# Kernel tuning notes

Measured on AMD Instinct MI355X. Metric: run time of the kernel, lower is better.

## Reference

```python
import jax, jax.numpy as jnp
import numpy as np

N_QUERY, N_POINTS, FEAT_DIM, K = 32768, 8192, 32, 8

def setup_inputs() -> dict:
    key = jax.random.key(0)
    k1, k2, k3 = jax.random.split(key, 3)
    xyz = jax.random.normal(k1, (N_QUERY, 3), dtype=jnp.float32)
    points = jax.random.normal(k2, (N_POINTS, 3), dtype=jnp.float32)
    # neural_point features are initialized uniform(-1e-4, 1e-4) in the module;
    # we use small-scale gaussians of the same magnitude.
    feats = jax.random.normal(k3, (N_POINTS, FEAT_DIM), dtype=jnp.float32) * 1e-4
    return {"xyz": xyz, "points": points, "feats": feats, "k": K}

def reference(xyz, points, feats, k):
    # Brute-force exact KNN (kpknn equivalent): squared euclidean distances [N, P]
    d2 = (jnp.sum(xyz * xyz, axis=-1, keepdims=True)
          - 2.0 * (xyz @ points.T)
          + jnp.sum(points * points, axis=-1)[None, :])
    _, idx = jax.lax.top_k(-d2, k)          # idx: [N, k] nearest-point indices
    knn_points = points[idx]                # [N, k, 3]
    knn_feats = feats[idx]                  # [N, k, FEAT_DIM]
    return knn_points, knn_feats
```

## Files before the change

kernel.cpp:

```cpp
#include <hip/hip_runtime.h>

#define NQ 32768
#define NP 8192
#define FD 32
#define KNN 8
#define QW 4
#define WPB 8
#define TB 512
#define QBLK (QW * WPB)
#define CHP 1024
#define NCH (NP / CHP)
#define ABLK 2048
#define CAP 128

typedef unsigned long long u64;

__device__ __forceinline__ u64 shfl_xor_u64(u64 k, int j) {
    unsigned lo = __shfl_xor((unsigned)k, j);
    unsigned hi = __shfl_xor((unsigned)(k >> 32), j);
    return ((u64)hi << 32) | lo;
}
__device__ __forceinline__ u64 sort64_u64(u64 key, int lane) {
    for (int k2 = 2; k2 <= 64; k2 <<= 1)
        for (int j = k2 >> 1; j > 0; j >>= 1) {
            u64 o = shfl_xor_u64(key, j);
            bool keepMin = ((lane & k2) == 0) == ((lane & j) == 0);
            key = ((o < key) == keepMin) ? o : key;
        }
    return key;
}
__device__ __forceinline__ float eighth_smallest64(float v, int lane) {
    for (int k2 = 2; k2 <= 64; k2 <<= 1)
        for (int j = k2 >> 1; j > 0; j >>= 1) {
            float o = __shfl_xor(v, j);
            bool keepMin = ((lane & k2) == 0) == ((lane & j) == 0);
            v = ((o < v) == keepMin) ? o : v;
        }
    return __uint_as_float((unsigned)__builtin_amdgcn_readlane((int)__float_as_uint(v), 7));
}

__global__ void k_prepack(const float* __restrict__ points, float4* __restrict__ pts4) {
    int i = blockIdx.x * blockDim.x + threadIdx.x;
    float px = points[i * 3 + 0], py = points[i * 3 + 1], pz = points[i * 3 + 2];
    float pn = __builtin_fmaf(pz, pz, __builtin_fmaf(py, py, px * px));
    pts4[i] = make_float4(-2.0f * px, -2.0f * py, -2.0f * pz, pn);
}

__global__ __launch_bounds__(TB) void knn_kernel(
    const float* __restrict__ xyz, const float* __restrict__ points,
    const float* __restrict__ feats, const float4* __restrict__ pts4,
    float* __restrict__ out)
{
#pragma clang fp contract(off)
    __shared__ float4 sp[CHP];
    __shared__ unsigned short sidx16[QBLK * CAP];
    __shared__ int scnt[QBLK];

    const int t     = threadIdx.x;
    const int lane  = t & 63;
    const int wid   = t >> 6;
    const int qbase = blockIdx.x * QBLK + wid * QW;

    if (t < QBLK) scnt[t] = 0;

    float qx[QW], qy[QW], qz[QW], qn[QW], mn[QW], tscr[QW];
#pragma unroll
    for (int qq = 0; qq < QW; ++qq) {
        int q = qbase + qq;
        float a = xyz[q * 3 + 0], b = xyz[q * 3 + 1], c = xyz[q * 3 + 2];
        qx[qq] = a; qy[qq] = b; qz[qq] = c;
        qn[qq] = (a * a + b * b) + c * c;
        mn[qq] = __builtin_inff();
    }

#pragma unroll 4
    for (int s = 0; s < ABLK / 64; ++s) {
        float4 p = pts4[s * 64 + lane];
#pragma unroll
        for (int qq = 0; qq < QW; ++qq) {
            float g = __builtin_fmaf(qx[qq], p.x,
                      __builtin_fmaf(qy[qq], p.y,
                      __builtin_fmaf(qz[qq], p.z, p.w)));
            mn[qq] = fminf(mn[qq], g);
        }
    }
#pragma unroll
    for (int qq = 0; qq < QW; ++qq)
        tscr[qq] = eighth_smallest64(mn[qq], lane) + 1e-3f;

    for (int c = 0; c < NCH; ++c) {
        __syncthreads();
        for (int i = t; i < CHP; i += TB) sp[i] = pts4[c * CHP + i];
        __syncthreads();
#pragma unroll 4
        for (int s = 0; s < CHP / 64; ++s) {
            float4 p = sp[s * 64 + lane];
#pragma unroll
            for (int qq = 0; qq < QW; ++qq) {
                float g = __builtin_fmaf(qx[qq], p.x,
                          __builtin_fmaf(qy[qq], p.y,
                          __builtin_fmaf(qz[qq], p.z, p.w)));
                if (__builtin_expect(g <= tscr[qq], 0)) {
                    int wq = wid * QW + qq;
                    int slot = atomicAdd(&scnt[wq], 1);
                    if (slot < CAP) sidx16[wq * CAP + slot] = (unsigned short)(c * CHP + s * 64 + lane);
                }
            }
        }
    }
    __syncthreads();

    const float4* feats4 = (const float4*)feats;
    float4* outf4 = (float4*)(out + (long)NQ * KNN * 3);
#pragma unroll 1
    for (int qq = 0; qq < QW; ++qq) {
        int wq = wid * QW + qq;
        int cnt = scnt[wq]; if (cnt > CAP) cnt = CAP;

        u64 key1 = ~0ull;
        if (lane < cnt) {
            int idx = sidx16[wq * CAP + lane];
            float px = points[idx * 3 + 0], py = points[idx * 3 + 1], pz = points[idx * 3 + 2];
            float pn  = (px * px + py * py) + pz * pz;
            float dot = __builtin_fmaf(qz[qq], pz, __builtin_fmaf(qy[qq], py, qx[qq] * px));
            float d2  = (qn[qq] - 2.0f * dot) + pn;
            unsigned b = __float_as_uint(d2);
            unsigned mk = (b & 0x80000000u) ? ~b : (b | 0x80000000u);
            key1 = ((u64)mk << 32) | (unsigned)idx;
        }
        u64 v = sort64_u64(key1, lane);

        if (cnt > 64) {
            u64 key2 = ~0ull;
            if (lane + 64 < cnt) {
                int idx = sidx16[wq * CAP + 64 + lane];
                float px = points[idx * 3 + 0], py = points[idx * 3 + 1], pz = points[idx * 3 + 2];
                float pn  = (px * px + py * py) + pz * pz;
                float dot = __builtin_fmaf(qz[qq], pz, __builtin_fmaf(qy[qq], py, qx[qq] * px));
                float d2  = (qn[qq] - 2.0f * dot) + pn;
                unsigned b = __float_as_uint(d2);
                unsigned mk = (b & 0x80000000u) ? ~b : (b | 0x80000000u);
                key2 = ((u64)mk << 32) | (unsigned)idx;
            }
            u64 s2 = sort64_u64(key2, lane);
            int src = (15 - lane) & 63;
            unsigned lo2 = __shfl((unsigned)s2, src);
            unsigned hi2 = __shfl((unsigned)(s2 >> 32), src);
            u64 kr = ((u64)hi2 << 32) | lo2;
            u64 m = (lane < 8) ? v : ((lane < 16) ? kr : ~0ull);
#pragma unroll
            for (int j = 8; j > 0; j >>= 1) {
                u64 o = shfl_xor_u64(m, j);
                bool low = (lane & j) == 0;
                m = low ? (o < m ? o : m) : (o < m ? m : o);
            }
            v = m;
        }

        int q = qbase + qq;
        int nb = __shfl((int)(unsigned)v, lane >> 3);
        outf4[(long)q * (KNN * FD / 4) + lane] = feats4[(long)nb * (FD / 4) + (lane & 7)];
        int j2 = lane / 3;
        int nb2 = __shfl((int)(unsigned)v, j2);
        if (lane < 24) {
            out[(long)q * (KNN * 3) + lane] = points[nb2 * 3 + (lane - j2 * 3)];
        }
    }
}

extern "C" void kernel_launch(void* const* d_in, const int* in_sizes, int n_in,
                              void* d_out, int out_size, void* d_ws, size_t ws_size,
                              hipStream_t stream) {
    const float* xyz    = (const float*)d_in[0];
    const float* points = (const float*)d_in[1];
    const float* feats  = (const float*)d_in[2];
    float* out = (float*)d_out;
    float4* pts4 = (float4*)d_ws;

    hipLaunchKernelGGL(k_prepack, dim3(NP / 256), dim3(256), 0, stream, points, pts4);
    hipLaunchKernelGGL(knn_kernel, dim3(NQ / QBLK), dim3(TB), 0, stream,
                       xyz, points, feats, pts4, out);
}
```

Before: 77.43 us.

## Compute KNN candidate distances with split-bf16 MFMA tiles instead of scalar FMAs

```diff
diff --git a/kernel.cpp b/kernel.cpp
--- a/kernel.cpp
+++ b/kernel.cpp
@@ -4,16 +4,26 @@
 #define NP 8192
 #define FD 32
 #define KNN 8
-#define QW 4
 #define WPB 8
 #define TB 512
-#define QBLK (QW * WPB)
-#define CHP 1024
-#define NCH (NP / CHP)
-#define ABLK 2048
+#define QBLK 32
+#define NTILE (NP / 16)
+#define QTILE (NTILE / 4)
+#define ATILE 32
 #define CAP 128
+#define MARGIN 1e-2f
 
 typedef unsigned long long u64;
+typedef short short8 __attribute__((ext_vector_type(8)));
+typedef float f32x4 __attribute__((ext_vector_type(4)));
+
+__device__ __forceinline__ unsigned short f2bf(float f) {
+    unsigned u = __float_as_uint(f);
+    return (unsigned short)((u + 0x7FFFu + ((u >> 16) & 1u)) >> 16);
+}
+__device__ __forceinline__ float bf2f(unsigned short s) {
+    return __uint_as_float(((unsigned)s) << 16);
+}
 
 __device__ __forceinline__ u64 shfl_xor_u64(u64 k, int j) {
     unsigned lo = __shfl_xor((unsigned)k, j);
@@ -39,71 +49,105 @@
     return __uint_as_float((unsigned)__builtin_amdgcn_readlane((int)__float_as_uint(v), 7));
 }
 
-__global__ void k_prepack(const float* __restrict__ points, float4* __restrict__ pts4) {
-    int i = blockIdx.x * blockDim.x + threadIdx.x;
+__global__ void k_prepack(const float* __restrict__ points, unsigned short* __restrict__ ptsB) {
+    int i = blockIdx.x * 256 + threadIdx.x;
     float px = points[i * 3 + 0], py = points[i * 3 + 1], pz = points[i * 3 + 2];
+    float mx = -2.0f * px, my = -2.0f * py, mz = -2.0f * pz;
     float pn = __builtin_fmaf(pz, pz, __builtin_fmaf(py, py, px * px));
-    pts4[i] = make_float4(-2.0f * px, -2.0f * py, -2.0f * pz, pn);
+    unsigned short mhx = f2bf(mx), mhy = f2bf(my), mhz = f2bf(mz);
+    unsigned short mlx = f2bf(mx - bf2f(mhx)), mly = f2bf(my - bf2f(mhy)), mlz = f2bf(mz - bf2f(mhz));
+    unsigned short pnh = f2bf(pn), pnl = f2bf(pn - bf2f(pnh));
+    unsigned s0 = (unsigned)mhx | ((unsigned)mhy << 16);
+    unsigned s1 = (unsigned)mhz | ((unsigned)mhx << 16);
+    unsigned s2 = (unsigned)mhy | ((unsigned)mhz << 16);
+    unsigned s3 = (unsigned)mlx | ((unsigned)mly << 16);
+    unsigned s4 = (unsigned)mlz | ((unsigned)pnh << 16);
+    unsigned s5 = (unsigned)pnl;
+    uint4* o = (uint4*)(ptsB + i * 16);
+    o[0] = make_uint4(s0, s1, s2, s3);
+    o[1] = make_uint4(s4, s5, 0u, 0u);
 }
 
 __global__ __launch_bounds__(TB) void knn_kernel(
     const float* __restrict__ xyz, const float* __restrict__ points,
-    const float* __restrict__ feats, const float4* __restrict__ pts4,
+    const float* __restrict__ feats, const unsigned short* __restrict__ ptsB,
     float* __restrict__ out)
 {
 #pragma clang fp contract(off)
-    __shared__ float4 sp[CHP];
+    __shared__ float smin[2][16][64];
+    __shared__ float stau[QBLK];
     __shared__ unsigned short sidx16[QBLK * CAP];
     __shared__ int scnt[QBLK];
 
-    const int t     = threadIdx.x;
-    const int lane  = t & 63;
-    const int wid   = t >> 6;
-    const int qbase = blockIdx.x * QBLK + wid * QW;
+    const int t = threadIdx.x, lane = t & 63, wid = t >> 6;
+    const int grp = wid >> 2, quarter = wid & 3;
+    const int col = lane & 15, kb = lane >> 4;
+    const int qbase_g = blockIdx.x * QBLK + grp * 16;
 
     if (t < QBLK) scnt[t] = 0;
 
-    float qx[QW], qy[QW], qz[QW], qn[QW], mn[QW], tscr[QW];
-#pragma unroll
-    for (int qq = 0; qq < QW; ++qq) {
-        int q = qbase + qq;
-        float a = xyz[q * 3 + 0], b = xyz[q * 3 + 1], c = xyz[q * 3 + 2];
-        qx[qq] = a; qy[qq] = b; qz[qq] = c;
-        qn[qq] = (a * a + b * b) + c * c;
-        mn[qq] = __builtin_inff();
-    }
-
+    short8 af = 0;
+    {
+        int qid = qbase_g + col;
+        float a = xyz[qid * 3 + 0], b = xyz[qid * 3 + 1], c = xyz[qid * 3 + 2];
+        unsigned short qhx = f2bf(a), qhy = f2bf(b), qhz = f2bf(c);
+        unsigned short qlx = f2bf(a - bf2f(qhx)), qly = f2bf(b - bf2f(qhy)), qlz = f2bf(c - bf2f(qhz));
+        if (kb == 0) {
+            af[0] = (short)qhx; af[1] = (short)qhy; af[2] = (short)qhz;
+            af[3] = (short)qlx; af[4] = (short)qly; af[5] = (short)qlz;
+            af[6] = (short)qhx; af[7] = (short)qhy;
+        } else if (kb == 1) {
+            af[0] = (short)qhz; af[1] = (short)0x3F80; af[2] = (short)0x3F80;
+        }
+    }
+
+    const int tb0 = quarter * QTILE;
+
+    f32x4 mnA;
+    mnA[0] = mnA[1] = mnA[2] = mnA[3] = __builtin_inff();
 #pragma unroll 4
-    for (int s = 0; s < ABLK / 64; ++s) {
-        float4 p = pts4[s * 64 + lane];
-#pragma unroll
-        for (int qq = 0; qq < QW; ++qq) {
-            float g = __builtin_fmaf(qx[qq], p.x,
-                      __builtin_fmaf(qy[qq], p.y,
-                      __builtin_fmaf(qz[qq], p.z, p.w)));
-            mn[qq] = fminf(mn[qq], g);
-        }
-    }
-#pragma unroll
-    for (int qq = 0; qq < QW; ++qq)
-        tscr[qq] = eighth_smallest64(mn[qq], lane) + 1e-3f;
-
-    for (int c = 0; c < NCH; ++c) {
-        __syncthreads();
-        for (int i = t; i < CHP; i += TB) sp[i] = pts4[c * CHP + i];
-        __syncthreads();
+    for (int s = 0; s < ATILE; ++s) {
+        int tb = tb0 + s;
+        short8 bf8 = 0;
+        if (kb < 2) bf8 = *(const short8*)(ptsB + tb * 256 + col * 16 + kb * 8);
+        f32x4 acc = {0.f, 0.f, 0.f, 0.f};
+        acc = __builtin_amdgcn_mfma_f32_16x16x32_bf16(af, bf8, acc, 0, 0, 0);
+#pragma unroll
+        for (int j = 0; j < 4; ++j) mnA[j] = fminf(mnA[j], acc[j]);
+    }
+#pragma unroll
+    for (int j = 0; j < 4; ++j) smin[grp][kb * 4 + j][quarter * 16 + col] = mnA[j];
+    __syncthreads();
+
+#pragma unroll
+    for (int j2 = 0; j2 < 4; ++j2) {
+        int qloc = wid * 4 + j2;
+        float v = smin[qloc >> 4][qloc & 15][lane];
+        float t8 = eighth_smallest64(v, lane);
+        if (lane == 0) stau[qloc] = t8 + MARGIN;
+    }
+    __syncthreads();
+    float tau4[4];
+#pragma unroll
+    for (int j = 0; j < 4; ++j) tau4[j] = stau[grp * 16 + kb * 4 + j];
+
 #pragma unroll 4
-        for (int s = 0; s < CHP / 64; ++s) {
-            float4 p = sp[s * 64 + lane];
-#pragma unroll
-            for (int qq = 0; qq < QW; ++qq) {
-                float g = __builtin_fmaf(qx[qq], p.x,
-                          __builtin_fmaf(qy[qq], p.y,
-                          __builtin_fmaf(qz[qq], p.z, p.w)));
-                if (__builtin_expect(g <= tscr[qq], 0)) {
-                    int wq = wid * QW + qq;
-                    int slot = atomicAdd(&scnt[wq], 1);
-                    if (slot < CAP) sidx16[wq * CAP + slot] = (unsigned short)(c * CHP + s * 64 + lane);
+    for (int s = 0; s < QTILE; ++s) {
+        int tb = tb0 + s;
+        short8 bf8 = 0;
+        if (kb < 2) bf8 = *(const short8*)(ptsB + tb * 256 + col * 16 + kb * 8);
+        f32x4 acc = {0.f, 0.f, 0.f, 0.f};
+        acc = __builtin_amdgcn_mfma_f32_16x16x32_bf16(af, bf8, acc, 0, 0, 0);
+        float d0 = acc[0] - tau4[0], d1 = acc[1] - tau4[1];
+        float d2 = acc[2] - tau4[2], d3 = acc[3] - tau4[3];
+        float dm = fminf(fminf(d0, d1), fminf(d2, d3));
+        if (__builtin_expect(dm <= 0.0f, 0)) {
+#pragma unroll
+            for (int j = 0; j < 4; ++j) {
+                if (acc[j] <= tau4[j]) {
+                    int qloc = grp * 16 + kb * 4 + j;
+                    int slot = atomicAdd(&scnt[qloc], 1);
+                    if (slot < CAP) sidx16[qloc * CAP + slot] = (unsigned short)(tb * 16 + col);
                 }
             }
         }
@@ -113,8 +157,11 @@
     const float4* feats4 = (const float4*)feats;
     float4* outf4 = (float4*)(out + (long)NQ * KNN * 3);
 #pragma unroll 1
-    for (int qq = 0; qq < QW; ++qq) {
-        int wq = wid * QW + qq;
+    for (int qq = 0; qq < 4; ++qq) {
+        int wq = wid * 4 + qq;
+        int q  = blockIdx.x * QBLK + wq;
+        float a = xyz[q * 3 + 0], b = xyz[q * 3 + 1], c = xyz[q * 3 + 2];
+        float qn = (a * a + b * b) + c * c;
         int cnt = scnt[wq]; if (cnt > CAP) cnt = CAP;
 
         u64 key1 = ~0ull;
@@ -122,10 +169,10 @@
             int idx = sidx16[wq * CAP + lane];
             float px = points[idx * 3 + 0], py = points[idx * 3 + 1], pz = points[idx * 3 + 2];
             float pn  = (px * px + py * py) + pz * pz;
-            float dot = __builtin_fmaf(qz[qq], pz, __builtin_fmaf(qy[qq], py, qx[qq] * px));
-            float d2  = (qn[qq] - 2.0f * dot) + pn;
-            unsigned b = __float_as_uint(d2);
-            unsigned mk = (b & 0x80000000u) ? ~b : (b | 0x80000000u);
+            float dot = __builtin_fmaf(c, pz, __builtin_fmaf(b, py, a * px));
+            float d2v = (qn - 2.0f * dot) + pn;
+            unsigned bb = __float_as_uint(d2v);
+            unsigned mk = (bb & 0x80000000u) ? ~bb : (bb | 0x80000000u);
             key1 = ((u64)mk << 32) | (unsigned)idx;
         }
         u64 v = sort64_u64(key1, lane);
@@ -136,10 +183,10 @@
                 int idx = sidx16[wq * CAP + 64 + lane];
                 float px = points[idx * 3 + 0], py = points[idx * 3 + 1], pz = points[idx * 3 + 2];
                 float pn  = (px * px + py * py) + pz * pz;
-                float dot = __builtin_fmaf(qz[qq], pz, __builtin_fmaf(qy[qq], py, qx[qq] * px));
-                float d2  = (qn[qq] - 2.0f * dot) + pn;
-                unsigned b = __float_as_uint(d2);
-                unsigned mk = (b & 0x80000000u) ? ~b : (b | 0x80000000u);
+                float dot = __builtin_fmaf(c, pz, __builtin_fmaf(b, py, a * px));
+                float d2v = (qn - 2.0f * dot) + pn;
+                unsigned bb = __float_as_uint(d2v);
+                unsigned mk = (bb & 0x80000000u) ? ~bb : (bb | 0x80000000u);
                 key2 = ((u64)mk << 32) | (unsigned)idx;
             }
             u64 s2 = sort64_u64(key2, lane);
@@ -157,7 +204,6 @@
             v = m;
         }
 
-        int q = qbase + qq;
         int nb = __shfl((int)(unsigned)v, lane >> 3);
         outf4[(long)q * (KNN * FD / 4) + lane] = feats4[(long)nb * (FD / 4) + (lane & 7)];
         int j2 = lane / 3;
@@ -175,9 +221,9 @@
     const float* points = (const float*)d_in[1];
     const float* feats  = (const float*)d_in[2];
     float* out = (float*)d_out;
-    float4* pts4 = (float4*)d_ws;
-
-    hipLaunchKernelGGL(k_prepack, dim3(NP / 256), dim3(256), 0, stream, points, pts4);
+    unsigned short* ptsB = (unsigned short*)d_ws;
+
+    hipLaunchKernelGGL(k_prepack, dim3(NP / 256), dim3(256), 0, stream, points, ptsB);
     hipLaunchKernelGGL(knn_kernel, dim3(NQ / QBLK), dim3(TB), 0, stream,
-                       xyz, points, feats, pts4, out);
-}
+                       xyz, points, feats, ptsB, out);
+}
```

Result: slower. 92.50 us (+19.5%).

## Double-buffer point chunks via global_load_lds and stage threshold pass through LDS

Applied to the files above, without the earlier changes.

```diff
diff --git a/kernel.cpp b/kernel.cpp
--- a/kernel.cpp
+++ b/kernel.cpp
@@ -8,9 +8,10 @@
 #define WPB 8
 #define TB 512
 #define QBLK (QW * WPB)
-#define CHP 1024
+#define CHP 512
+#define ACH 4
 #define NCH (NP / CHP)
-#define ABLK 2048
+#define NC (ACH + NCH)
 #define CAP 128
 
 typedef unsigned long long u64;
@@ -52,7 +53,7 @@
     float* __restrict__ out)
 {
 #pragma clang fp contract(off)
-    __shared__ float4 sp[CHP];
+    __shared__ float4 spbuf[2][CHP];
     __shared__ unsigned short sidx16[QBLK * CAP];
     __shared__ int scnt[QBLK];
 
@@ -71,50 +72,69 @@
         qx[qq] = a; qy[qq] = b; qz[qq] = c;
         qn[qq] = (a * a + b * b) + c * c;
         mn[qq] = __builtin_inff();
+        tscr[qq] = __builtin_inff();
     }
 
-#pragma unroll 4
-    for (int s = 0; s < ABLK / 64; ++s) {
-        float4 p = pts4[s * 64 + lane];
-#pragma unroll
-        for (int qq = 0; qq < QW; ++qq) {
-            float g = __builtin_fmaf(qx[qq], p.x,
-                      __builtin_fmaf(qy[qq], p.y,
-                      __builtin_fmaf(qz[qq], p.z, p.w)));
-            mn[qq] = fminf(mn[qq], g);
-        }
+#define STAGE(cid, bb)                                                              \
+    __builtin_amdgcn_global_load_lds(                                               \
+        (const __attribute__((address_space(1))) void*)(pts4 + (cid) * CHP + t),    \
+        (__attribute__((address_space(3))) void*)(&spbuf[bb][t]), 16, 0, 0)
+
+    STAGE(0, 0);
+    __syncthreads();
+
+    for (int c = 0; c < NC; ++c) {
+        int b = c & 1;
+        if (c + 1 < NC) {
+            int nk = c + 1;
+            STAGE(nk < ACH ? nk : nk - ACH, nk & 1);
+        }
+        if (c < ACH) {
+#pragma unroll
+            for (int s = 0; s < CHP / 64; ++s) {
+                float4 p = spbuf[b][s * 64 + lane];
+#pragma unroll
+                for (int qq = 0; qq < QW; ++qq) {
+                    float g = __builtin_fmaf(qx[qq], p.x,
+                              __builtin_fmaf(qy[qq], p.y,
+                              __builtin_fmaf(qz[qq], p.z, p.w)));
+                    mn[qq] = fminf(mn[qq], g);
+                }
+            }
+            if (c == ACH - 1) {
+#pragma unroll
+                for (int qq = 0; qq < QW; ++qq)
+                    tscr[qq] = eighth_smallest64(mn[qq], lane) + 1e-3f;
+            }
+        } else {
+            int cid = c - ACH;
+#pragma unroll
+            for (int s = 0; s < CHP / 64; ++s) {
+                float4 p = spbuf[b][s * 64 + lane];
+                int gidx = cid * CHP + s * 64 + lane;
+#pragma unroll
+                for (int qq = 0; qq < QW; ++qq) {
+                    float g = __builtin_fmaf(qx[qq], p.x,
+                              __builtin_fmaf(qy[qq], p.y,
+                              __builtin_fmaf(qz[qq], p.z, p.w)));
+                    if (__builtin_expect(g <= tscr[qq], 0)) {
+                        int wq = wid * QW + qq;
+                        int slot = atomicAdd(&scnt[wq], 1);
+                        if (slot < CAP) sidx16[wq * CAP + slot] = (unsigned short)gidx;
+                    }
+                }
+            }
+        }
+        __syncthreads();
     }
-#pragma unroll
-    for (int qq = 0; qq < QW; ++qq)
-        tscr[qq] = eighth_smallest64(mn[qq], lane) + 1e-3f;
-
-    for (int c = 0; c < NCH; ++c) {
-        __syncthreads();
-        for (int i = t; i < CHP; i += TB) sp[i] = pts4[c * CHP + i];
-        __syncthreads();
-#pragma unroll 4
-        for (int s = 0; s < CHP / 64; ++s) {
-            float4 p = sp[s * 64 + lane];
-#pragma unroll
-            for (int qq = 0; qq < QW; ++qq) {
-                float g = __builtin_fmaf(qx[qq], p.x,
-                          __builtin_fmaf(qy[qq], p.y,
-                          __builtin_fmaf(qz[qq], p.z, p.w)));
-                if (__builtin_expect(g <= tscr[qq], 0)) {
-                    int wq = wid * QW + qq;
-                    int slot = atomicAdd(&scnt[wq], 1);
-                    if (slot < CAP) sidx16[wq * CAP + slot] = (unsigned short)(c * CHP + s * 64 + lane);
-                }
-            }
-        }
-    }
-    __syncthreads();
+#undef STAGE
 
     const float4* feats4 = (const float4*)feats;
     float4* outf4 = (float4*)(out + (long)NQ * KNN * 3);
 #pragma unroll 1
     for (int qq = 0; qq < QW; ++qq) {
         int wq = wid * QW + qq;
+        int q  = qbase + qq;
         int cnt = scnt[wq]; if (cnt > CAP) cnt = CAP;
 
         u64 key1 = ~0ull;
@@ -123,9 +143,9 @@
             float px = points[idx * 3 + 0], py = points[idx * 3 + 1], pz = points[idx * 3 + 2];
             float pn  = (px * px + py * py) + pz * pz;
             float dot = __builtin_fmaf(qz[qq], pz, __builtin_fmaf(qy[qq], py, qx[qq] * px));
-            float d2  = (qn[qq] - 2.0f * dot) + pn;
-            unsigned b = __float_as_uint(d2);
-            unsigned mk = (b & 0x80000000u) ? ~b : (b | 0x80000000u);
+            float d2v = (qn[qq] - 2.0f * dot) + pn;
+            unsigned bb = __float_as_uint(d2v);
+            unsigned mk = (bb & 0x80000000u) ? ~bb : (bb | 0x80000000u);
             key1 = ((u64)mk << 32) | (unsigned)idx;
         }
         u64 v = sort64_u64(key1, lane);
@@ -137,9 +157,9 @@
                 float px = points[idx * 3 + 0], py = points[idx * 3 + 1], pz = points[idx * 3 + 2];
                 float pn  = (px * px + py * py) + pz * pz;
                 float dot = __builtin_fmaf(qz[qq], pz, __builtin_fmaf(qy[qq], py, qx[qq] * px));
-                float d2  = (qn[qq] - 2.0f * dot) + pn;
-                unsigned b = __float_as_uint(d2);
-                unsigned mk = (b & 0x80000000u) ? ~b : (b | 0x80000000u);
+                float d2v = (qn[qq] - 2.0f * dot) + pn;
+                unsigned bb = __float_as_uint(d2v);
+                unsigned mk = (bb & 0x80000000u) ? ~bb : (bb | 0x80000000u);
                 key2 = ((u64)mk << 32) | (unsigned)idx;
             }
             u64 s2 = sort64_u64(key2, lane);
@@ -157,7 +177,6 @@
             v = m;
         }
 
-        int q = qbase + qq;
         int nb = __shfl((int)(unsigned)v, lane >> 3);
         outf4[(long)q * (KNN * FD / 4) + lane] = feats4[(long)nb * (FD / 4) + (lane & 7)];
         int j2 = lane / 3;
```

Result: no change. 78.49 us (+1.4%).
